# Performance work log

Measured on AMD Instinct MI355X. Metric: run time of the kernel, lower is better.

## Reference

```python
import jax, jax.numpy as jnp
import numpy as np

N_BITS = 32
HIDDEN = 128


def _neighborhoods(z):
    """z: (B,k,H,W) -> (B,k,9,H,W) 3x3 neighborhoods (zero-padded), center zeroed.

    Position ordering matches F.unfold(kernel_size=3): row-major over (di,dj),
    so index 4 is the center, which the module masks to 0.
    """
    B, k, H, W = z.shape
    zp = jnp.pad(z, ((0, 0), (0, 0), (1, 1), (1, 1)))
    views = []
    for di in range(3):
        for dj in range(3):
            if di == 1 and dj == 1:  # center masked out
                views.append(jnp.zeros_like(z))
            else:
                views.append(zp[:, :, di:di + H, dj:dj + W])
    return jnp.stack(views, axis=2)  # (B,k,9,H,W)


def setup_inputs() -> dict:
    key = jax.random.key(0)
    k1, k2, k3, k4, k5 = jax.random.split(key, 5)
    B, k, H, W = 8, N_BITS, 256, 256
    z = jax.random.normal(k1, (B, k, H, W), dtype=jnp.float32)
    # nn.Linear(9*k, hidden): weight (hidden, 9k), feature order = k-outer, 9-inner
    W1 = jax.random.normal(k2, (HIDDEN, 9 * k), dtype=jnp.float32) * (1.0 / np.sqrt(9 * k))
    b1 = jax.random.normal(k3, (HIDDEN,), dtype=jnp.float32) * 0.01
    W2 = jax.random.normal(k4, (k, HIDDEN), dtype=jnp.float32) * (1.0 / np.sqrt(HIDDEN))
    b2 = jax.random.normal(k5, (k,), dtype=jnp.float32) * 0.01
    return {"z": z, "W1": W1, "b1": b1, "W2": W2, "b2": b2}


def reference(z, W1, b1, W2, b2):
    B, k, H, W = z.shape
    win = _neighborhoods(z)                      # (B,k,9,H,W)
    W1r = W1.reshape(HIDDEN, k, 9)               # split (9k) -> (k,9), k-outer
    h = jnp.einsum('bkphw,dkp->bdhw', win, W1r) + b1[None, :, None, None]
    h = jax.nn.relu(h)
    logits = jnp.einsum('bdhw,kd->bkhw', h, W2) + b2[None, :, None, None]
    return logits  # (B,k,H,W)
```

## Files before the change

### kernel.cpp

```cpp
#include <hip/hip_runtime.h>


#define KC 32
#define HH 256
#define WW 256
#define HID 128
#define YS 8
#define ZROW 2640

typedef __attribute__((ext_vector_type(8))) short short8;
typedef __attribute__((ext_vector_type(4))) float f32x4;

#define BARRIER() asm volatile("s_waitcnt lgkmcnt(0)\n\ts_barrier" ::: "memory")
#define SCHED_FENCE() asm volatile("" ::: "memory")

__device__ __forceinline__ unsigned short f2bf(float f) {
    union { float f; unsigned int i; } x; x.f = f;
    unsigned int r = x.i + 0x7FFFu + ((x.i >> 16) & 1u);
    return (unsigned short)(r >> 16);
}

__device__ __forceinline__ short8 pack8(const float* v) {
    union { short8 s; unsigned int u[4]; } w;
    union { float f; unsigned int i; } uu[8];
#pragma unroll
    for (int j = 0; j < 8; ++j) uu[j].f = v[j];
#pragma unroll
    for (int k = 0; k < 4; ++k)
        w.u[k] = __builtin_amdgcn_perm(uu[2 * k + 1].i, uu[2 * k].i, 0x07060302u);
    return w.s;
}

__global__ void prep_weights(const float* __restrict__ w1,
                             const float* __restrict__ w2,
                             unsigned short* __restrict__ w1t,
                             unsigned short* __restrict__ w2t) {
    int i = blockIdx.x * 256 + threadIdx.x;
    if (i < 9 * HID * KC) {
        int c = i & 31;
        int d = (i >> 5) & 127;
        int p = i >> 12;
        w1t[i] = f2bf(w1[d * (9 * KC) + c * 9 + p]);
    } else if (i < 9 * HID * KC + KC * HID) {
        int j = i - 9 * HID * KC;
        w2t[j] = f2bf(w2[j]);
    }
}

__global__ __launch_bounds__(256, 4) void local_pred_kernel(
    const float* __restrict__ zg,
    const unsigned short* __restrict__ w1t,
    const float* __restrict__ b1g,
    const unsigned short* __restrict__ w2t,
    const float* __restrict__ b2g,
    float* __restrict__ outg)
{
    __shared__ __attribute__((aligned(16))) unsigned short z_lds[4 * ZROW];
    __shared__ __attribute__((aligned(16))) unsigned short h_lds[64 * 136];
    __shared__ __attribute__((aligned(16))) unsigned short halo_lds[7 * 2 * 32];

    const int tid  = threadIdx.x;
    const int bidx = blockIdx.x;
    const int x0 = (bidx & 3) << 6;
    const int y0 = ((bidx >> 2) & 31) * YS;
    const int b  = bidx >> 7;

    const int l = tid & 63;
    const int o = tid >> 6;

    const int wave = tid >> 6;
    const int lane = tid & 63;
    const int lr = lane & 15;
    const int lq = lane >> 4;

    const float* zb = zg + (size_t)b * KC * HH * WW;

    float p8[3][8];
#pragma unroll
    for (int dy = 0; dy < 3; ++dy) {
        const int gy = y0 - 1 + dy;
        const bool ok = (unsigned)gy < (unsigned)HH;
        const int gyc = ok ? gy : 0;
        const float* p = zb + ((size_t)(o * 8) * HH + gyc) * WW + x0 + l;
#pragma unroll
        for (int j = 0; j < 8; ++j) p8[dy][j] = ok ? p[(size_t)j * HH * WW] : 0.f;
    }
    const int nhs = tid & 1, nho = (tid >> 1) & 3, nhd = tid >> 3;
    float nh8[8];
    {
        const int gy = y0 - 1 + nhd;
        const int gx = x0 - 1 + nhs * 65;
        const bool ok = (tid < 24) && ((unsigned)gy < (unsigned)HH) &&
                        ((unsigned)gx < (unsigned)WW);
        const int gyc = ok ? gy : 0, gxc = ok ? gx : 0;
        const float* q = zb + ((size_t)(nho * 8) * HH + gyc) * WW + gxc;
#pragma unroll
        for (int j = 0; j < 8; ++j) nh8[j] = ok ? q[(size_t)j * HH * WW] : 0.f;
    }
    const int fidx = tid - 64;
    const int fhs = fidx & 1, fho = (fidx >> 1) & 3, fhr = fidx >> 3;
    float fh8[8];
    {
        const int gy = y0 + 2 + fhr;
        const int gx = x0 - 1 + fhs * 65;
        const bool ok = (tid >= 64) && (tid < 120) && (gy < HH) &&
                        ((unsigned)gx < (unsigned)WW);
        const int gyc = ok ? gy : 0, gxc = ok ? gx : 0;
        const float* q = zb + ((size_t)(fho * 8) * HH + gyc) * WW + gxc;
#pragma unroll
        for (int j = 0; j < 8; ++j) fh8[j] = ok ? q[(size_t)j * HH * WW] : 0.f;
    }
    float mv[2][8];
    {
        const float* p = zb + ((size_t)(o * 8) * HH + (y0 + 2)) * WW + x0 + l;
#pragma unroll
        for (int j = 0; j < 8; ++j) mv[0][j] = p[(size_t)j * HH * WW];
    }
#pragma unroll
    for (int dy = 0; dy < 3; ++dy)
        *(short8*)&z_lds[(dy * 66 + l + 1) * 40 + o * 8] = pack8(p8[dy]);
    if (tid < 24)
        *(short8*)&z_lds[(nhd * 66 + nhs * 65) * 40 + nho * 8] = pack8(nh8);
    if (tid >= 64 && tid < 120)
        *(short8*)&halo_lds[(fhr * 2 + fhs) * 32 + fho * 8] = pack8(fh8);

    float bias1[2], bias2[2];
#pragma unroll
    for (int nt = 0; nt < 2; ++nt) bias1[nt] = b1g[wave * 32 + nt * 16 + lr];
#pragma unroll
    for (int nt = 0; nt < 2; ++nt) bias2[nt] = b2g[nt * 16 + lr];
    short8 w2f[4][2];
#pragma unroll
    for (int k4 = 0; k4 < 4; ++k4)
#pragma unroll
        for (int nt = 0; nt < 2; ++nt)
            w2f[k4][nt] = *(const short8*)&w2t[(nt * 16 + lr) * HID + k4 * 32 + lq * 8];

    BARRIER();

    const int tap_di[8] = {0, 0, 0, 1, 1, 2, 2, 2};
    const int tap_dj[8] = {0, 1, 2, 0, 2, 0, 1, 2};

#pragma unroll
    for (int r = 0; r < YS; ++r) {
        const int y = y0 + r;
        const int S0 = r & 3, S1 = (r + 1) & 3, S2 = (r + 2) & 3, S3 = (r + 3) & 3;

        f32x4 acc[4][2];
#pragma unroll
        for (int mt = 0; mt < 4; ++mt)
#pragma unroll
            for (int nt = 0; nt < 2; ++nt)
                acc[mt][nt] = (f32x4){0.f, 0.f, 0.f, 0.f};

        const int rowoff[3] = {S0 * ZROW, S1 * ZROW, S2 * ZROW};
#pragma unroll
        for (int t = 0; t < 8; ++t) {
            const int di = tap_di[t], dj = tap_dj[t];
            const int p = di * 3 + dj;
            short8 afr[4];
#pragma unroll
            for (int mt = 0; mt < 4; ++mt)
                afr[mt] = *(const short8*)&z_lds[rowoff[di] + (mt * 16 + lr + dj) * 40 + lq * 8];
            short8 bfr[2];
#pragma unroll
            for (int nt = 0; nt < 2; ++nt)
                bfr[nt] = *(const short8*)&w1t[p * (HID * KC) + (wave * 32 + nt * 16 + lr) * KC + lq * 8];
#pragma unroll
            for (int nt = 0; nt < 2; ++nt)
#pragma unroll
                for (int mt = 0; mt < 4; ++mt)
                    acc[mt][nt] = __builtin_amdgcn_mfma_f32_16x16x32_bf16(
                        afr[mt], bfr[nt], acc[mt][nt], 0, 0, 0);
        }

        SCHED_FENCE();
        if (r < 6) {
            const int gy = y + 3;
            const bool ok = gy < HH;
            const int gyc = ok ? gy : 0;
            const float* p = zb + ((size_t)(o * 8) * HH + gyc) * WW + x0 + l;
#pragma unroll
            for (int j = 0; j < 8; ++j) mv[(r + 1) & 1][j] = ok ? p[(size_t)j * HH * WW] : 0.f;
        }
        SCHED_FENCE();

#pragma unroll
        for (int nt = 0; nt < 2; ++nt) {
            const int d = wave * 32 + nt * 16 + lr;
#pragma unroll
            for (int mt = 0; mt < 4; ++mt)
#pragma unroll
                for (int rr = 0; rr < 4; ++rr) {
                    float v = acc[mt][nt][rr] + bias1[nt];
                    v = v > 0.f ? v : 0.f;
                    const int m = mt * 16 + lq * 4 + rr;
                    h_lds[m * 136 + d] = f2bf(v);
                }
        }
        BARRIER();

        f32x4 acc2[2];
        acc2[0] = (f32x4){0.f, 0.f, 0.f, 0.f};
        acc2[1] = (f32x4){0.f, 0.f, 0.f, 0.f};
        const int m2 = wave * 16 + lr;
#pragma unroll
        for (int k4 = 0; k4 < 4; ++k4) {
            short8 afr = *(const short8*)&h_lds[m2 * 136 + k4 * 32 + lq * 8];
#pragma unroll
            for (int nt = 0; nt < 2; ++nt)
                acc2[nt] = __builtin_amdgcn_mfma_f32_16x16x32_bf16(
                    afr, w2f[k4][nt], acc2[nt], 0, 0, 0);
        }

#pragma unroll
        for (int nt = 0; nt < 2; ++nt) {
            const int kout = nt * 16 + lr;
            f32x4 pk;
#pragma unroll
            for (int rr = 0; rr < 4; ++rr) pk[rr] = acc2[nt][rr] + bias2[nt];
            const int mb = wave * 16 + lq * 4;
            const size_t off = ((size_t)(b * KC + kout) * HH + y) * WW + x0 + mb;
            *(f32x4*)&outg[off] = pk;
        }

        if (r < 7) {
            *(short8*)&z_lds[(S3 * 66 + l + 1) * 40 + o * 8] = pack8(mv[r & 1]);
            if (tid < 8) {
                const int side = tid & 1, oct = tid >> 1;
                short8 hv = *(const short8*)&halo_lds[(r * 2 + side) * 32 + oct * 8];
                *(short8*)&z_lds[(S3 * 66 + side * 65) * 40 + oct * 8] = hv;
            }
        }
        BARRIER();
    }
}

extern "C" void kernel_launch(void* const* d_in, const int* in_sizes, int n_in,
                              void* d_out, int out_size, void* d_ws, size_t ws_size,
                              hipStream_t stream)
{
    const float* z  = (const float*)d_in[0];
    const float* W1 = (const float*)d_in[1];
    const float* b1 = (const float*)d_in[2];
    const float* W2 = (const float*)d_in[3];
    const float* b2 = (const float*)d_in[4];
    float* out = (float*)d_out;
    unsigned short* w1t = (unsigned short*)d_ws;
    unsigned short* w2t = (unsigned short*)d_ws + 9 * HID * KC;

    hipLaunchKernelGGL(prep_weights, dim3(160), dim3(256), 0, stream, W1, W2, w1t, w2t);
    hipLaunchKernelGGL(local_pred_kernel, dim3(8 * 4 * (HH / YS)), dim3(256), 0, stream,
                       z, w1t, b1, w2t, b2, out);
}
```

Baseline: 210.5 us.

## Cut register pressure: single-buffer row prefetch, reload W2 fragments, relax launch bounds

Reduces VGPR usage by storing each prologue load into LDS right after it arrives instead of holding all of them in registers. The next-row prefetch changes from a double buffer loaded after the MFMA loop to a single buffer loaded at the top of each row iteration. W2 fragments are reloaded from global memory inside the second GEMM rather than kept in registers. The launch-bounds occupancy hint drops from 4 to 3 blocks. The prefetch now has less time to complete before it is needed, the W2 reloads add global traffic on every row, and the relaxed hint may allow lower occupancy.

```diff
diff --git a/kernel.cpp b/kernel.cpp
--- a/kernel.cpp
+++ b/kernel.cpp
@@ -47,7 +47,7 @@
     }
 }
 
-__global__ __launch_bounds__(256, 4) void local_pred_kernel(
+__global__ __launch_bounds__(256, 3) void local_pred_kernel(
     const float* __restrict__ zg,
     const unsigned short* __restrict__ w1t,
     const float* __restrict__ b1g,
@@ -75,76 +75,74 @@
 
     const float* zb = zg + (size_t)b * KC * HH * WW;
 
-    float p8[3][8];
 #pragma unroll
     for (int dy = 0; dy < 3; ++dy) {
         const int gy = y0 - 1 + dy;
         const bool ok = (unsigned)gy < (unsigned)HH;
         const int gyc = ok ? gy : 0;
         const float* p = zb + ((size_t)(o * 8) * HH + gyc) * WW + x0 + l;
-#pragma unroll
-        for (int j = 0; j < 8; ++j) p8[dy][j] = ok ? p[(size_t)j * HH * WW] : 0.f;
-    }
-    const int nhs = tid & 1, nho = (tid >> 1) & 3, nhd = tid >> 3;
-    float nh8[8];
+        float t8[8];
+#pragma unroll
+        for (int j = 0; j < 8; ++j) t8[j] = ok ? p[(size_t)j * HH * WW] : 0.f;
+        *(short8*)&z_lds[(dy * 66 + l + 1) * 40 + o * 8] = pack8(t8);
+        SCHED_FENCE();
+    }
     {
-        const int gy = y0 - 1 + nhd;
-        const int gx = x0 - 1 + nhs * 65;
+        const int s = tid & 1, oc = (tid >> 1) & 3, dy = tid >> 3;
+        const int gy = y0 - 1 + dy;
+        const int gx = x0 - 1 + s * 65;
         const bool ok = (tid < 24) && ((unsigned)gy < (unsigned)HH) &&
                         ((unsigned)gx < (unsigned)WW);
-        const int gyc = ok ? gy : 0, gxc = ok ? gx : 0;
-        const float* q = zb + ((size_t)(nho * 8) * HH + gyc) * WW + gxc;
-#pragma unroll
-        for (int j = 0; j < 8; ++j) nh8[j] = ok ? q[(size_t)j * HH * WW] : 0.f;
-    }
-    const int fidx = tid - 64;
-    const int fhs = fidx & 1, fho = (fidx >> 1) & 3, fhr = fidx >> 3;
-    float fh8[8];
+        const float* q = zb + ((size_t)(oc * 8) * HH + (ok ? gy : 0)) * WW + (ok ? gx : 0);
+        float t8[8];
+#pragma unroll
+        for (int j = 0; j < 8; ++j) t8[j] = ok ? q[(size_t)j * HH * WW] : 0.f;
+        if (tid < 24)
+            *(short8*)&z_lds[(dy * 66 + s * 65) * 40 + oc * 8] = pack8(t8);
+        SCHED_FENCE();
+    }
     {
-        const int gy = y0 + 2 + fhr;
-        const int gx = x0 - 1 + fhs * 65;
+        const int fi = tid - 64;
+        const int s = fi & 1, oc = (fi >> 1) & 3, fr = fi >> 3;
+        const int gy = y0 + 2 + fr;
+        const int gx = x0 - 1 + s * 65;
         const bool ok = (tid >= 64) && (tid < 120) && (gy < HH) &&
                         ((unsigned)gx < (unsigned)WW);
-        const int gyc = ok ? gy : 0, gxc = ok ? gx : 0;
-        const float* q = zb + ((size_t)(fho * 8) * HH + gyc) * WW + gxc;
-#pragma unroll
-        for (int j = 0; j < 8; ++j) fh8[j] = ok ? q[(size_t)j * HH * WW] : 0.f;
-    }
-    float mv[2][8];
-    {
-        const float* p = zb + ((size_t)(o * 8) * HH + (y0 + 2)) * WW + x0 + l;
-#pragma unroll
-        for (int j = 0; j < 8; ++j) mv[0][j] = p[(size_t)j * HH * WW];
-    }
-#pragma unroll
-    for (int dy = 0; dy < 3; ++dy)
-        *(short8*)&z_lds[(dy * 66 + l + 1) * 40 + o * 8] = pack8(p8[dy]);
-    if (tid < 24)
-        *(short8*)&z_lds[(nhd * 66 + nhs * 65) * 40 + nho * 8] = pack8(nh8);
-    if (tid >= 64 && tid < 120)
-        *(short8*)&halo_lds[(fhr * 2 + fhs) * 32 + fho * 8] = pack8(fh8);
+        const float* q = zb + ((size_t)(oc * 8) * HH + (ok ? gy : 0)) * WW + (ok ? gx : 0);
+        float t8[8];
+#pragma unroll
+        for (int j = 0; j < 8; ++j) t8[j] = ok ? q[(size_t)j * HH * WW] : 0.f;
+        if (tid >= 64 && tid < 120)
+            *(short8*)&halo_lds[(fr * 2 + s) * 32 + oc * 8] = pack8(t8);
+        SCHED_FENCE();
+    }
 
     float bias1[2], bias2[2];
 #pragma unroll
     for (int nt = 0; nt < 2; ++nt) bias1[nt] = b1g[wave * 32 + nt * 16 + lr];
 #pragma unroll
     for (int nt = 0; nt < 2; ++nt) bias2[nt] = b2g[nt * 16 + lr];
-    short8 w2f[4][2];
-#pragma unroll
-    for (int k4 = 0; k4 < 4; ++k4)
-#pragma unroll
-        for (int nt = 0; nt < 2; ++nt)
-            w2f[k4][nt] = *(const short8*)&w2t[(nt * 16 + lr) * HID + k4 * 32 + lq * 8];
 
     BARRIER();
 
     const int tap_di[8] = {0, 0, 0, 1, 1, 2, 2, 2};
     const int tap_dj[8] = {0, 1, 2, 0, 2, 0, 1, 2};
+
+    float mv8[8];
 
 #pragma unroll
     for (int r = 0; r < YS; ++r) {
         const int y = y0 + r;
         const int S0 = r & 3, S1 = (r + 1) & 3, S2 = (r + 2) & 3, S3 = (r + 3) & 3;
+
+        if (r < 7) {
+            const int gy = y + 2;
+            const bool ok = gy < HH;
+            const float* p = zb + ((size_t)(o * 8) * HH + (ok ? gy : 0)) * WW + x0 + l;
+#pragma unroll
+            for (int j = 0; j < 8; ++j) mv8[j] = ok ? p[(size_t)j * HH * WW] : 0.f;
+        }
+        SCHED_FENCE();
 
         f32x4 acc[4][2];
 #pragma unroll
@@ -173,17 +171,6 @@
                     acc[mt][nt] = __builtin_amdgcn_mfma_f32_16x16x32_bf16(
                         afr[mt], bfr[nt], acc[mt][nt], 0, 0, 0);
         }
-
-        SCHED_FENCE();
-        if (r < 6) {
-            const int gy = y + 3;
-            const bool ok = gy < HH;
-            const int gyc = ok ? gy : 0;
-            const float* p = zb + ((size_t)(o * 8) * HH + gyc) * WW + x0 + l;
-#pragma unroll
-            for (int j = 0; j < 8; ++j) mv[(r + 1) & 1][j] = ok ? p[(size_t)j * HH * WW] : 0.f;
-        }
-        SCHED_FENCE();
 
 #pragma unroll
         for (int nt = 0; nt < 2; ++nt) {
@@ -208,9 +195,10 @@
         for (int k4 = 0; k4 < 4; ++k4) {
             short8 afr = *(const short8*)&h_lds[m2 * 136 + k4 * 32 + lq * 8];
 #pragma unroll
-            for (int nt = 0; nt < 2; ++nt)
-                acc2[nt] = __builtin_amdgcn_mfma_f32_16x16x32_bf16(
-                    afr, w2f[k4][nt], acc2[nt], 0, 0, 0);
+            for (int nt = 0; nt < 2; ++nt) {
+                short8 bfr = *(const short8*)&w2t[(nt * 16 + lr) * HID + k4 * 32 + lq * 8];
+                acc2[nt] = __builtin_amdgcn_mfma_f32_16x16x32_bf16(afr, bfr, acc2[nt], 0, 0, 0);
+            }
         }
 
 #pragma unroll
@@ -225,7 +213,7 @@
         }
 
         if (r < 7) {
-            *(short8*)&z_lds[(S3 * 66 + l + 1) * 40 + o * 8] = pack8(mv[r & 1]);
+            *(short8*)&z_lds[(S3 * 66 + l + 1) * 40 + o * 8] = pack8(mv8);
             if (tid < 8) {
                 const int side = tid & 1, oct = tid >> 1;
                 short8 hv = *(const short8*)&halo_lds[(r * 2 + side) * 32 + oct * 8];
```

Result: faster. 174.9 us (-16.9%).
